# Optimization experiments

Hardware: AMD Instinct MI355X
Metric: run time of the kernel (lower is better)

The kernel has to match this reference:

```python
import jax, jax.numpy as jnp
import numpy as np

SIG_G = [1, 1, 1]          # Clifford signature Cl(3,0): 2^3 = 8 blades
N_BLADES = 1 << len(SIG_G)
LAYER_DIMS = [256, 512, 256]
BATCH = 64
ALPHA = 0.1


def _cayley(g):
    """Cayley table C[a,b,k]: e_a * e_b = C[a,b,a^b] * e_{a^b} (blades as bitmasks)."""
    n = len(g)
    K = 1 << n
    C = np.zeros((K, K, K), dtype=np.float32)
    for a in range(K):
        for b in range(K):
            # canonical reordering sign: count generator swaps
            s, aa = 0, a >> 1
            while aa:
                s += bin(aa & b).count('1')
                aa >>= 1
            sign = -1.0 if (s & 1) else 1.0
            # metric contraction for repeated generators
            for i in range(n):
                if (a >> i) & 1 and (b >> i) & 1:
                    sign *= g[i]
            C[a, b, a ^ b] = sign
    return C


def _reverse_signs(n):
    """Reversion sign per blade: (-1)^{r(r-1)/2} for grade r."""
    K = 1 << n
    r = np.array([bin(k).count('1') for k in range(K)])
    return ((-1.0) ** (r * (r - 1) // 2)).astype(np.float32)


CAYLEY = jnp.asarray(_cayley(SIG_G))          # (K, K, K), sparse signed table
REV = jnp.asarray(_reverse_signs(len(SIG_G)))  # (K,)


def geometric_product(A, W, C):
    # A: (B, N, K) multivectors, W: (M, N, K) multivector weights -> (B, M, K)
    # out[b,m,k] = sum_n sum_{a,c} C[a,c,k] * A[b,n,a] * W[m,n,c]
    return jnp.einsum('bna,mnc,ack->bmk', A, W, C)


def setup_inputs() -> dict:
    key = jax.random.key(0)
    k_x, k_w1, k_w2 = jax.random.split(key, 3)
    x = jax.random.normal(k_x, (BATCH, LAYER_DIMS[0], N_BLADES), dtype=jnp.float32)
    w1 = jax.random.normal(k_w1, (LAYER_DIMS[0], LAYER_DIMS[1], N_BLADES), dtype=jnp.float32) * 0.1
    w2 = jax.random.normal(k_w2, (LAYER_DIMS[1], LAYER_DIMS[2], N_BLADES), dtype=jnp.float32) * 0.1
    return {"x": x, "w1": w1, "w2": w2, "n_iter": 20}


def reference(x, w1, w2, n_iter):
    ws = [w1, w2]
    B = x.shape[0]
    # states[0] is detached input (x.detach().clone() in torch)
    states = [jax.lax.stop_gradient(x)]
    for w in ws:
        states.append(jnp.zeros((B, w.shape[1], N_BLADES), dtype=x.dtype))
    for _ in range(n_iter):
        for l in range(1, len(states)):
            w = ws[l - 1]
            x_hat = geometric_product(states[l], w, CAYLEY)          # (B, D_{l-1}, K)
            err = states[l - 1] - x_hat
            w_T = jnp.transpose(w * REV, (1, 0, 2))                  # reverse + transpose
            # torch: grad = -gp(err, w_T); states[l] -= alpha*grad  => += alpha*gp
            states[l] = states[l] + ALPHA * geometric_product(err, w_T, CAYLEY)
    return tuple(states)
```

## Files before the change

kernel.cpp:

```cpp
#include <hip/hip_runtime.h>

typedef unsigned short u16;
typedef __attribute__((ext_vector_type(4))) float f32x4;
typedef __attribute__((ext_vector_type(8))) __bf16 bf16x8;
typedef __attribute__((ext_vector_type(8))) u16 u16x8;

#define ALPHA_F 0.1f

__device__ __host__ constexpr bool SGN(int a, int c) {
  return ((((c & 1) & (((a >> 1) ^ (a >> 2)) & 1)) ^
           (((c >> 1) & 1) & ((a >> 2) & 1))) != 0);
}
__device__ __host__ constexpr float REVF(int c) {
  const int r = (c & 1) + ((c >> 1) & 1) + ((c >> 2) & 1);
  return (r >= 2) ? -1.f : 1.f;
}
__device__ __forceinline__ u16 bf_rnd(float f) {
  unsigned u = __float_as_uint(f);
  return (u16)((u + 0x7FFFu + ((u >> 16) & 1u)) >> 16);
}
__device__ __forceinline__ float bf_val(u16 h) {
  return __uint_as_float(((unsigned)h) << 16);
}
__device__ __forceinline__ f32x4 mf(bf16x8 a, bf16x8 b, f32x4 c) {
  return __builtin_amdgcn_mfma_f32_16x16x32_bf16(a, b, c, 0, 0, 0);
}
__device__ __forceinline__ bf16x8 negf(bf16x8 v) {
  u16x8 u = __builtin_bit_cast(u16x8, v);
  const u16x8 m = {0x8000, 0x8000, 0x8000, 0x8000, 0x8000, 0x8000, 0x8000, 0x8000};
  u = u ^ m;
  return __builtin_bit_cast(bf16x8, u);
}

__global__ __launch_bounds__(256) void pack_in(
    const float* __restrict__ x, const float* __restrict__ w1,
    const float* __restrict__ w2, u16* P1h, u16* P1l, u16* Q1, u16* Qc1,
    u16* P2h, u16* P2l, u16* Q2, u16* Axh, u16* Axl, u16* Vpk2,
    u16* BpAh, u16* BpAl, u16* Z0h, u16* Z0l, float* out0) {
  const int t = blockIdx.x * 256 + threadIdx.x;
  if (t < 131072) {
    const int r = t >> 9, cc = t & 511;
    const float* s = w1 + ((size_t)r * 512 + cc) * 8;
    float v[8];
#pragma unroll
    for (int c = 0; c < 8; ++c) v[c] = s[c];
    const size_t qo = (size_t)((cc >> 4) * 2 + (r >> 7)) * 32768 +
                      ((r >> 5) & 3) * 512 + ((r >> 3) & 3) * 128 +
                      (cc & 15) * 8 + (r & 7);
#pragma unroll
    for (int c = 0; c < 8; ++c) {
      const float q1 = REVF(c) * v[c];
      u16 h = bf_rnd(q1);
      Q1[qo + c * 4096] = h;
      Q1[qo + c * 4096 + 2048] = bf_rnd(q1 - bf_val(h));
      const float qc = ALPHA_F * q1;
      h = bf_rnd(qc);
      Qc1[qo + c * 4096] = h;
      Qc1[qo + c * 4096 + 2048] = bf_rnd(qc - bf_val(h));
    }
  } else if (t < 262144) {
    const int u = t - 131072;
    const int r = u >> 8, c2 = u & 255;
    const float* s = w2 + ((size_t)r * 256 + c2) * 8;
    float v[8];
#pragma unroll
    for (int c = 0; c < 8; ++c) v[c] = s[c];
    const size_t tail = ((r >> 5) & 3) * 512 + ((r >> 3) & 3) * 128 +
                        (c2 & 15) * 8 + (r & 7);
    const size_t qo = (size_t)((c2 >> 4) * 4 + (r >> 7)) * 32768 + tail;
    const size_t wo = (size_t)((c2 >> 4) * 6 + 2 + (r >> 7)) * 32768 + tail;
#pragma unroll
    for (int c = 0; c < 8; ++c) {
      const float q2 = REVF(c) * v[c];
      u16 h = bf_rnd(q2);
      Q2[qo + c * 4096] = h;
      Q2[qo + c * 4096 + 2048] = bf_rnd(q2 - bf_val(h));
      const float qw = ALPHA_F * q2;
      h = bf_rnd(qw);
      const u16 lo = bf_rnd(qw - bf_val(h));
      Vpk2[wo + c * 4096] = h;
      Vpk2[wo + c * 4096 + 2048] = lo;
      const size_t bo = ((size_t)(c * 32 + (c2 >> 3)) * 512 + r) * 8 + (c2 & 7);
      BpAh[bo] = h;
      BpAl[bo] = lo;
    }
  } else if (t < 393216) {
    const int u = t - 262144;
    const int r = u & 255, cc = u >> 8;
    const float* s = w1 + ((size_t)r * 512 + cc) * 8;
#pragma unroll
    for (int a = 0; a < 8; ++a) {
      const float v = s[a];
      const u16 h = bf_rnd(v);
      const size_t o = ((size_t)(a * 32 + (r >> 3)) * 512 + cc) * 8 + (r & 7);
      P1h[o] = h;
      P1l[o] = bf_rnd(v - bf_val(h));
    }
  } else if (t < 524288) {
    const int u = t - 393216;
    const int r = u & 511, c2 = u >> 9;
    const float* s = w2 + ((size_t)r * 256 + c2) * 8;
#pragma unroll
    for (int a = 0; a < 8; ++a) {
      const float v = s[a];
      const u16 h = bf_rnd(v);
      const size_t o = ((size_t)(a * 64 + (r >> 3)) * 256 + c2) * 8 + (r & 7);
      P2h[o] = h;
      P2l[o] = bf_rnd(v - bf_val(h));
    }
  } else if (t < 540672) {
    const int u = t - 524288;
    const int b = u >> 8, n = u & 255;
    const float* s = x + ((size_t)b * 256 + n) * 8;
#pragma unroll
    for (int a = 0; a < 8; ++a) {
      const u16 h = bf_rnd(s[a]);
      const size_t o = ((size_t)(a * 32 + (n >> 3)) * 64 + b) * 8 + (n & 7);
      Axh[o] = h;
      Axl[o] = bf_rnd(s[a] - bf_val(h));
    }
  } else if (t < 573440) {
    const int u = t - 540672;
    ((float4*)out0)[u] = ((const float4*)x)[u];
  } else if (t < 606208) {
    const int u = t - 573440;
    const int hl = u >> 14, i = u & 16383;
    const int a = i >> 11, j = i & 2047;
    const u16x8 z = {0, 0, 0, 0, 0, 0, 0, 0};
    u16* Z = hl ? Z0l : Z0h;
    *(u16x8*)&Z[(size_t)a * 49152 + (size_t)j * 8] = z;
  }
}

__global__ __launch_bounds__(512, 2) void composeK(
    const u16* __restrict__ P1h, const u16* __restrict__ P1l,
    const u16* __restrict__ Q1, const u16* __restrict__ P2h,
    const u16* __restrict__ P2l, const u16* __restrict__ Q2,
    const u16* __restrict__ Axh, const u16* __restrict__ Axl,
    const u16* __restrict__ Qc1, u16* Vpk1, u16* Vpk2,
    u16* V1pAh, u16* V1pAl, u16* UpAh, u16* UpAl,
    u16* Z0h, u16* Z0l, float* c1Z) {
  __shared__ float pan[8][2176];

  const int bid = blockIdx.x, tid = threadIdx.x;
  const int w = tid >> 6, l = tid & 63;
  const int lg = l >> 4, lm = l & 15;

  int seg, rb, p;
  if (bid < 256) { seg = 1; rb = bid & 15; p = bid >> 4; }
  else if (bid < 1280) { seg = 0; rb = (bid - 256) & 31; p = (bid - 256) >> 5; }
  else { seg = 2; rb = (bid - 1280) & 3; p = (bid - 1280) >> 2; }

  const u16* Ah_ = seg == 0 ? P1h : (seg == 1 ? P2h : Axh);
  const u16* Al_ = seg == 0 ? P1l : (seg == 1 ? P2l : Axl);
  const u16* Vb = seg == 0 ? Q1 : (seg == 1 ? Q2 : Qc1);
  const int NROW = seg == 0 ? 512 : (seg == 1 ? 256 : 64);
  const int KC = seg == 1 ? 64 : 32;
  const int NW = seg == 1 ? 2 : 1;
  const int slmul = seg == 1 ? 4 : 2;
  const int row = rb * 16 + lm;

  f32x4 acc[8];
#pragma unroll
  for (int k = 0; k < 8; ++k) acc[k] = f32x4{0.f, 0.f, 0.f, 0.f};

  for (int wi = 0; wi < NW; ++wi) {
    const int n0 = w * (NW * 32) + wi * 32;
    const int sl = n0 >> 7, hst = (n0 >> 5) & 3;
    const u16* Vimg =
        Vb + ((size_t)(p * slmul + sl) << 15) + hst * 512 + lg * 128 + lm * 8;
    const int kc = (n0 >> 3) + lg;
    bf16x8 ah[8], al[8];
#pragma unroll
    for (int a = 0; a < 8; ++a) {
      const size_t o = ((size_t)(a * KC + kc) * NROW + row) * 8;
      ah[a] = *(const bf16x8*)(Ah_ + o);
      al[a] = *(const bf16x8*)(Al_ + o);
    }
    __builtin_amdgcn_s_setprio(1);
#pragma unroll
    for (int c = 0; c < 8; ++c) {
      const bf16x8 vhp = *(const bf16x8*)(Vimg + (size_t)c * 4096);
      const bf16x8 vlp = *(const bf16x8*)(Vimg + (size_t)c * 4096 + 2048);
      const bf16x8 vhn = negf(vhp), vln = negf(vlp);
#pragma unroll
      for (int a = 0; a < 8; ++a) {
        const int k = a ^ c;
        const bf16x8 vh = SGN(a, c) ? vhn : vhp;
        const bf16x8 vl = SGN(a, c) ? vln : vlp;
        acc[k] = mf(ah[a], vh, acc[k]);
        acc[k] = mf(al[a], vh, acc[k]);
        acc[k] = mf(ah[a], vl, acc[k]);
      }
    }
    __builtin_amdgcn_s_setprio(0);
  }

#pragma unroll
  for (int k = 0; k < 8; ++k)
#pragma unroll
    for (int q = 0; q < 4; ++q)
      pan[w][(k * 16 + lg * 4 + q) * 17 + lm] = acc[k][q];
  __syncthreads();

  if (tid < 256) {
    const int k = tid >> 5, rw = (tid >> 1) & 15, ch = tid & 1;
    const int boff = (k * 16 + rw) * 17 + ch * 8;
    f32x4 s0 = {0.f, 0.f, 0.f, 0.f}, s1 = {0.f, 0.f, 0.f, 0.f};
    for (int ss = 0; ss < 8; ++ss) {
      s0 += *(const f32x4*)&pan[ss][boff];
      s1 += *(const f32x4*)&pan[ss][boff + 4];
    }
    float v[8];
#pragma unroll
    for (int e = 0; e < 4; ++e) { v[e] = s0[e]; v[4 + e] = s1[e]; }
    const int n = rb * 16 + rw;

    if (seg <= 1) {
      u16* base = seg == 0 ? Vpk1 : Vpk2;
      const int blk = (seg == 0 ? p * 4 : p * 6) + (n >> 7);
      u16* d = base + ((size_t)blk << 15) + (size_t)k * 4096 +
               ((n >> 5) & 3) * 512 + ((n >> 3) & 3) * 128 + (n & 7);
      u16 ph[8], pl[8];
#pragma unroll
      for (int e = 0; e < 8; ++e) {
        const int m = p * 16 + ch * 8 + e;
        const float val = ((k == 0) && (n == m) ? 1.0f : 0.0f) - ALPHA_F * v[e];
        const u16 hh = bf_rnd(val);
        const u16 ll = bf_rnd(val - bf_val(hh));
        d[(size_t)(ch * 8 + e) * 8] = hh;
        d[2048 + (size_t)(ch * 8 + e) * 8] = ll;
        ph[e] = hh;
        pl[e] = ll;
      }
      if (seg == 0) {
        const size_t po = (((size_t)k * 64 + p * 2 + ch) * 512 + n) * 8;
        *(u16x8*)&V1pAh[po] = *(u16x8*)ph;
        *(u16x8*)&V1pAl[po] = *(u16x8*)pl;
      } else {
        const size_t po = (((size_t)k * 32 + p * 2 + ch) * 256 + n) * 8;
        *(u16x8*)&UpAh[po] = *(u16x8*)ph;
        *(u16x8*)&UpAl[po] = *(u16x8*)pl;
      }
    } else {
      const int b = n;
      float* cp_ = c1Z + (((size_t)k * 64 + p * 2 + ch) * 64 + b) * 8;
      u16x8 h8, l8;
#pragma unroll
      for (int e = 0; e < 8; ++e) {
        cp_[e] = v[e];
        const u16 hh = bf_rnd(v[e]);
        h8[e] = hh;
        l8[e] = bf_rnd(v[e] - bf_val(hh));
      }
      const size_t zo = (((size_t)k * 96 + 32 + p * 2 + ch) * 64 + b) * 8;
      *(u16x8*)&Z0h[zo] = h8;
      *(u16x8*)&Z0l[zo] = l8;
    }
  }
}

__global__ __launch_bounds__(512, 2) void compose2(
    const u16* __restrict__ V1pAh, const u16* __restrict__ V1pAl,
    const u16* __restrict__ UpAh, const u16* __restrict__ UpAl,
    const u16* __restrict__ BpAh, const u16* __restrict__ BpAl,
    const u16* __restrict__ Vpk1, const u16* __restrict__ Wcat,
    u16* V1sqI, u16* Wcat2) {
  __shared__ float pan[8][2176];

  const int bid = blockIdx.x, tid = threadIdx.x;
  const int w = tid >> 6, l = tid & 63;
  const int lg = l >> 4, lm = l & 15;

  int seg, rb, p;
  if (bid < 1024) { seg = 0; rb = bid & 31; p = bid >> 5; }
  else if (bid < 1536) { seg = 1; rb = (bid - 1024) & 31; p = (bid - 1024) >> 5; }
  else { seg = 2; rb = (bid - 1536) & 15; p = (bid - 1536) >> 4; }

  const int nwin = seg == 0 ? 2 : (seg == 1 ? 3 : 1);
  const int row = rb * 16 + lm;

  f32x4 acc[8];
#pragma unroll
  for (int k = 0; k < 8; ++k) acc[k] = f32x4{0.f, 0.f, 0.f, 0.f};

  for (int wi = 0; wi < nwin; ++wi) {
    const int g = w * nwin + wi;
    const u16 *Aph, *Apl;
    int AKC, AR, kcb;
    const u16* Vimg;
    if (seg == 0) {
      Aph = V1pAh; Apl = V1pAl; AKC = 64; AR = 512; kcb = g * 4;
      Vimg = Vpk1 + ((size_t)(p * 4 + (g >> 2)) << 15) + (g & 3) * 512;
    } else if (seg == 1) {
      if (g < 8) {
        Aph = BpAh; Apl = BpAl; AKC = 32; AR = 512; kcb = g * 4;
        Vimg = Wcat + ((size_t)(p * 6 + (g >> 2)) << 15) + (g & 3) * 512;
      } else {
        const int g2_ = g - 8;
        Aph = V1pAh; Apl = V1pAl; AKC = 64; AR = 512; kcb = g2_ * 4;
        Vimg = Wcat + ((size_t)(p * 6 + 2 + (g2_ >> 2)) << 15) + (g2_ & 3) * 512;
      }
    } else {
      Aph = UpAh; Apl = UpAl; AKC = 32; AR = 256; kcb = g * 4;
      Vimg = Wcat + ((size_t)(p * 6 + (g >> 2)) << 15) + (g & 3) * 512;
    }
    Vimg += lg * 128 + lm * 8;
    const int kc = kcb + lg;
    bf16x8 ah[8], al[8];
#pragma unroll
    for (int a = 0; a < 8; ++a) {
      const size_t o = ((size_t)(a * AKC + kc) * AR + row) * 8;
      ah[a] = *(const bf16x8*)(Aph + o);
      al[a] = *(const bf16x8*)(Apl + o);
    }
    __builtin_amdgcn_s_setprio(1);
#pragma unroll
    for (int c = 0; c < 8; ++c) {
      const bf16x8 vhp = *(const bf16x8*)(Vimg + (size_t)c * 4096);
      const bf16x8 vlp = *(const bf16x8*)(Vimg + (size_t)c * 4096 + 2048);
      const bf16x8 vhn = negf(vhp), vln = negf(vlp);
#pragma unroll
      for (int a = 0; a < 8; ++a) {
        const int k = a ^ c;
        const bf16x8 vh = SGN(a, c) ? vhn : vhp;
        const bf16x8 vl = SGN(a, c) ? vln : vlp;
        acc[k] = mf(ah[a], vh, acc[k]);
        acc[k] = mf(al[a], vh, acc[k]);
        acc[k] = mf(ah[a], vl, acc[k]);
      }
    }
    __builtin_amdgcn_s_setprio(0);
  }

#pragma unroll
  for (int k = 0; k < 8; ++k)
#pragma unroll
    for (int q = 0; q < 4; ++q)
      pan[w][(k * 16 + lg * 4 + q) * 17 + lm] = acc[k][q];
  __syncthreads();

  if (tid < 256) {
    const int k = tid >> 5, rw = (tid >> 1) & 15, ch = tid & 1;
    const int boff = (k * 16 + rw) * 17 + ch * 8;
    f32x4 s0 = {0.f, 0.f, 0.f, 0.f}, s1 = {0.f, 0.f, 0.f, 0.f};
    for (int ss = 0; ss < 8; ++ss) {
      s0 += *(const f32x4*)&pan[ss][boff];
      s1 += *(const f32x4*)&pan[ss][boff + 4];
    }
    float v[8];
#pragma unroll
    for (int e = 0; e < 4; ++e) { v[e] = s0[e]; v[4 + e] = s1[e]; }
    const int n = rb * 16 + rw;

    u16* base = seg == 0 ? V1sqI : Wcat2;
    int blk;
    if (seg == 0) blk = p * 4 + (n >> 7);
    else if (seg == 1) blk = p * 6 + 2 + (n >> 7);
    else blk = p * 6 + (n >> 7);
    u16* d = base + ((size_t)blk << 15) + (size_t)k * 4096 +
             ((n >> 5) & 3) * 512 + ((n >> 3) & 3) * 128 + (n & 7);
#pragma unroll
    for (int e = 0; e < 8; ++e) {
      const float val = v[e];
      const u16 hh = bf_rnd(val);
      d[(size_t)(ch * 8 + e) * 8] = hh;
      d[2048 + (size_t)(ch * 8 + e) * 8] = bf_rnd(val - bf_val(hh));
    }
  }
}

struct IArgs {
  const u16 *Zch, *Zcl;
  u16 *Znh, *Znl;
  const u16 *V1, *V2;
  const float *add1, *add2;
  float *oa1, *oa2;
  float *out1, *out2;
  int n_g1;
};

template <bool G1>
__device__ __forceinline__ void iter_body(const IArgs& A, int t18, int fin,
                                          float (*pan)[2176]) {
  const int bid = blockIdx.x, tid = threadIdx.x;
  const int w = tid >> 6, l = tid & 63;
  const int lg = l >> 4, lm = l & 15;
  const int rb = G1 ? bid : bid - A.n_g1;
  constexpr int NPAN = G1 ? 32 : 16;
  const int p = rb & (NPAN - 1);
  const int bh = rb / NPAN;
  const int b0 = bh * 16;
  constexpr int KW = G1 ? 64 : 96;
  constexpr int NW = G1 ? 2 : 3;
  constexpr int acb0 = G1 ? 32 : 0;
  constexpr int slmul = G1 ? 4 : 6;
  const u16* Vb = G1 ? A.V1 : A.V2;

  f32x4 acc[8];
#pragma unroll
  for (int k = 0; k < 8; ++k) acc[k] = f32x4{0.f, 0.f, 0.f, 0.f};

#pragma unroll
  for (int wi = 0; wi < NW; ++wi) {
    const int n0 = w * KW + wi * 32;
    const int sl = n0 >> 7, hst = (n0 >> 5) & 3;
    const u16* Vimg = Vb + ((size_t)(p * slmul + sl) << 15) + hst * 512 +
                      lg * 128 + lm * 8;
    const size_t ao = ((size_t)(acb0 + (n0 >> 3) + lg) * 64 + b0 + lm) * 8;
    bf16x8 ah[8], al[8];
#pragma unroll
    for (int a = 0; a < 8; ++a) {
      ah[a] = *(const bf16x8*)(A.Zch + (size_t)a * 49152 + ao);
      al[a] = *(const bf16x8*)(A.Zcl + (size_t)a * 49152 + ao);
    }
    __builtin_amdgcn_s_setprio(1);
#pragma unroll
    for (int c = 0; c < 8; ++c) {
      const bf16x8 vhp = *(const bf16x8*)(Vimg + (size_t)c * 4096);
      const bf16x8 vlp = *(const bf16x8*)(Vimg + (size_t)c * 4096 + 2048);
      const bf16x8 vhn = negf(vhp), vln = negf(vlp);
#pragma unroll
      for (int a = 0; a < 8; ++a) {
        const int k = a ^ c;
        const bf16x8 vh = SGN(a, c) ? vhn : vhp;
        const bf16x8 vl = SGN(a, c) ? vln : vlp;
        acc[k] = mf(ah[a], vh, acc[k]);
        acc[k] = mf(al[a], vh, acc[k]);
        acc[k] = mf(ah[a], vl, acc[k]);
      }
    }
    __builtin_amdgcn_s_setprio(0);
  }

#pragma unroll
  for (int k = 0; k < 8; ++k)
#pragma unroll
    for (int q = 0; q < 4; ++q)
      pan[w][(k * 16 + lg * 4 + q) * 17 + lm] = acc[k][q];
  __syncthreads();

  if (tid < 256) {
    const int k = tid >> 5, row = (tid >> 1) & 15, ch = tid & 1;
    const int boff = (k * 16 + row) * 17 + ch * 8;
    f32x4 s0 = {0.f, 0.f, 0.f, 0.f}, s1 = {0.f, 0.f, 0.f, 0.f};
    for (int ss = 0; ss < 8; ++ss) {
      s0 += *(const f32x4*)&pan[ss][boff];
      s1 += *(const f32x4*)&pan[ss][boff + 4];
    }
    const int b = b0 + row;
    if constexpr (G1) {
      if (A.add1) {
        const float* ca = A.add1 + (((size_t)k * 64 + p * 2 + ch) * 64 + b) * 8;
        s0 += *(const f32x4*)ca;
        s1 += *(const f32x4*)(ca + 4);
      }
    } else {
      if (A.add2) {
        const float* ca = A.add2 + (((size_t)k * 32 + p * 2 + ch) * 64 + b) * 8;
        s0 += *(const f32x4*)ca;
        s1 += *(const f32x4*)(ca + 4);
      }
    }
    float v[8];
#pragma unroll
    for (int e = 0; e < 4; ++e) { v[e] = s0[e]; v[4 + e] = s1[e]; }
    if constexpr (G1) {
      if (A.oa1) {
        float* q = A.oa1 + (((size_t)k * 64 + p * 2 + ch) * 64 + b) * 8;
#pragma unroll
        for (int e = 0; e < 8; ++e) q[e] = v[e];
      }
    } else {
      if (A.oa2) {
        float* q = A.oa2 + (((size_t)k * 32 + p * 2 + ch) * 64 + b) * 8;
#pragma unroll
        for (int e = 0; e < 8; ++e) q[e] = v[e];
      }
    }
    if (!fin) {
      u16x8 h8, l8;
#pragma unroll
      for (int e = 0; e < 8; ++e) {
        const u16 hh = bf_rnd(v[e]);
        h8[e] = hh;
        l8[e] = bf_rnd(v[e] - bf_val(hh));
      }
      const size_t zo =
          (((size_t)k * 96 + (G1 ? 32 : 0) + p * 2 + ch) * 64 + b) * 8;
      *(u16x8*)&A.Znh[zo] = h8;
      *(u16x8*)&A.Znl[zo] = l8;
    }
    if constexpr (G1) {
      if (t18) {
#pragma unroll
        for (int e = 0; e < 8; ++e)
          A.out1[((size_t)b * 512 + p * 16 + ch * 8 + e) * 8 + k] = v[e];
      }
    } else {
      if (fin) {
#pragma unroll
        for (int e = 0; e < 8; ++e)
          A.out2[((size_t)b * 256 + p * 16 + ch * 8 + e) * 8 + k] = v[e];
      }
    }
  }
}

__global__ __launch_bounds__(512, 2) void iter_k(IArgs A, int t18, int fin) {
  __shared__ float pan[8][2176];
  if ((int)blockIdx.x < A.n_g1) iter_body<true>(A, t18, fin, pan);
  else iter_body<false>(A, t18, fin, pan);
}

extern "C" void kernel_launch(void* const* d_in, const int* in_sizes, int n_in,
                              void* d_out, int out_size, void* d_ws,
                              size_t ws_size, hipStream_t stream) {
  const float* x = (const float*)d_in[0];
  const float* w1 = (const float*)d_in[1];
  const float* w2 = (const float*)d_in[2];

  float* out0 = (float*)d_out;
  float* out1 = out0 + 131072;
  float* out2 = out1 + 262144;

  char* W = (char*)d_ws;
  const size_t MB = 1ull << 20;
  u16* Vpk1 = (u16*)(W);
  u16* Wcat = (u16*)(W + 8 * MB);
  u16* Q1 = (u16*)(W + 14 * MB);
  u16* Q2 = (u16*)(W + 18 * MB);
  u16* Qc1 = (u16*)(W + 22 * MB);
  u16* P1h = (u16*)(W + 26 * MB);
  u16* P1l = (u16*)(W + 28 * MB);
  u16* P2h = (u16*)(W + 30 * MB);
  u16* P2l = (u16*)(W + 32 * MB);
  u16* Axh = (u16*)(W + 34 * MB);
  u16* Axl = (u16*)(W + 34 * MB + 262144);
  float* c1Z = (float*)(W + 35 * MB);
  u16* V1sqI = (u16*)(W + 36 * MB);
  u16* Wcat2 = (u16*)(W + 44 * MB);
  u16* V1pAh = (u16*)(W + 50 * MB);
  u16* V1pAl = (u16*)(W + 54 * MB);
  u16* UpAh = (u16*)(W + 58 * MB);
  u16* UpAl = (u16*)(W + 59 * MB);
  u16* BpAh = (u16*)(W + 60 * MB);
  u16* BpAl = (u16*)(W + 62 * MB);
  float* c1bZ = (float*)(W + 64 * MB);
  float* d2Z = (float*)(W + 65 * MB);
  u16* Z0h = (u16*)(W + 66 * MB);
  u16* Z0l = Z0h + 393216;
  u16* Z1h = Z0h + 786432;
  u16* Z1l = Z0h + 1179648;

  pack_in<<<2368, 256, 0, stream>>>(x, w1, w2, P1h, P1l, Q1, Qc1, P2h, P2l, Q2,
                                    Axh, Axl, Wcat, BpAh, BpAl, Z0h, Z0l, out0);

  composeK<<<1408, 512, 0, stream>>>(P1h, P1l, Q1, P2h, P2l, Q2, Axh, Axl, Qc1,
                                     Vpk1, Wcat, V1pAh, V1pAl, UpAh, UpAl,
                                     Z0h, Z0l, c1Z);

  compose2<<<1792, 512, 0, stream>>>(V1pAh, V1pAl, UpAh, UpAl, BpAh, BpAl,
                                     Vpk1, Wcat, V1sqI, Wcat2);

  {
    IArgs ia{Z0h, Z0l, Z1h, Z1l, Vpk1, Wcat, c1Z, nullptr,
             c1bZ, d2Z, out1, out2, 128};
    iter_k<<<192, 512, 0, stream>>>(ia, 0, 0);
  }

  for (int tau = 0; tau < 9; ++tau) {
    const bool odd = tau & 1;
    IArgs ia{odd ? Z0h : Z1h, odd ? Z0l : Z1l,
             odd ? Z1h : Z0h, odd ? Z1l : Z0l,
             V1sqI, Wcat2, c1bZ, d2Z, nullptr, nullptr, out1, out2, 128};
    iter_k<<<192, 512, 0, stream>>>(ia, tau == 8 ? 1 : 0, 0);
  }

  {
    IArgs ia{Z0h, Z0l, Z1h, Z1l, Vpk1, Wcat, nullptr, nullptr,
             nullptr, nullptr, out1, out2, 0};
    iter_k<<<64, 512, 0, stream>>>(ia, 0, 1);
  }
}
```

Before: 363.0 us.

## Fuse compose2 with first iteration kernel and double row tile for seg0

```diff
diff --git a/kernel.cpp b/kernel.cpp
--- a/kernel.cpp
+++ b/kernel.cpp
@@ -260,116 +260,6 @@
   }
 }
 
-__global__ __launch_bounds__(512, 2) void compose2(
-    const u16* __restrict__ V1pAh, const u16* __restrict__ V1pAl,
-    const u16* __restrict__ UpAh, const u16* __restrict__ UpAl,
-    const u16* __restrict__ BpAh, const u16* __restrict__ BpAl,
-    const u16* __restrict__ Vpk1, const u16* __restrict__ Wcat,
-    u16* V1sqI, u16* Wcat2) {
-  __shared__ float pan[8][2176];
-
-  const int bid = blockIdx.x, tid = threadIdx.x;
-  const int w = tid >> 6, l = tid & 63;
-  const int lg = l >> 4, lm = l & 15;
-
-  int seg, rb, p;
-  if (bid < 1024) { seg = 0; rb = bid & 31; p = bid >> 5; }
-  else if (bid < 1536) { seg = 1; rb = (bid - 1024) & 31; p = (bid - 1024) >> 5; }
-  else { seg = 2; rb = (bid - 1536) & 15; p = (bid - 1536) >> 4; }
-
-  const int nwin = seg == 0 ? 2 : (seg == 1 ? 3 : 1);
-  const int row = rb * 16 + lm;
-
-  f32x4 acc[8];
-#pragma unroll
-  for (int k = 0; k < 8; ++k) acc[k] = f32x4{0.f, 0.f, 0.f, 0.f};
-
-  for (int wi = 0; wi < nwin; ++wi) {
-    const int g = w * nwin + wi;
-    const u16 *Aph, *Apl;
-    int AKC, AR, kcb;
-    const u16* Vimg;
-    if (seg == 0) {
-      Aph = V1pAh; Apl = V1pAl; AKC = 64; AR = 512; kcb = g * 4;
-      Vimg = Vpk1 + ((size_t)(p * 4 + (g >> 2)) << 15) + (g & 3) * 512;
-    } else if (seg == 1) {
-      if (g < 8) {
-        Aph = BpAh; Apl = BpAl; AKC = 32; AR = 512; kcb = g * 4;
-        Vimg = Wcat + ((size_t)(p * 6 + (g >> 2)) << 15) + (g & 3) * 512;
-      } else {
-        const int g2_ = g - 8;
-        Aph = V1pAh; Apl = V1pAl; AKC = 64; AR = 512; kcb = g2_ * 4;
-        Vimg = Wcat + ((size_t)(p * 6 + 2 + (g2_ >> 2)) << 15) + (g2_ & 3) * 512;
-      }
-    } else {
-      Aph = UpAh; Apl = UpAl; AKC = 32; AR = 256; kcb = g * 4;
-      Vimg = Wcat + ((size_t)(p * 6 + (g >> 2)) << 15) + (g & 3) * 512;
-    }
-    Vimg += lg * 128 + lm * 8;
-    const int kc = kcb + lg;
-    bf16x8 ah[8], al[8];
-#pragma unroll
-    for (int a = 0; a < 8; ++a) {
-      const size_t o = ((size_t)(a * AKC + kc) * AR + row) * 8;
-      ah[a] = *(const bf16x8*)(Aph + o);
-      al[a] = *(const bf16x8*)(Apl + o);
-    }
-    __builtin_amdgcn_s_setprio(1);
-#pragma unroll
-    for (int c = 0; c < 8; ++c) {
-      const bf16x8 vhp = *(const bf16x8*)(Vimg + (size_t)c * 4096);
-      const bf16x8 vlp = *(const bf16x8*)(Vimg + (size_t)c * 4096 + 2048);
-      const bf16x8 vhn = negf(vhp), vln = negf(vlp);
-#pragma unroll
-      for (int a = 0; a < 8; ++a) {
-        const int k = a ^ c;
-        const bf16x8 vh = SGN(a, c) ? vhn : vhp;
-        const bf16x8 vl = SGN(a, c) ? vln : vlp;
-        acc[k] = mf(ah[a], vh, acc[k]);
-        acc[k] = mf(al[a], vh, acc[k]);
-        acc[k] = mf(ah[a], vl, acc[k]);
-      }
-    }
-    __builtin_amdgcn_s_setprio(0);
-  }
-
-#pragma unroll
-  for (int k = 0; k < 8; ++k)
-#pragma unroll
-    for (int q = 0; q < 4; ++q)
-      pan[w][(k * 16 + lg * 4 + q) * 17 + lm] = acc[k][q];
-  __syncthreads();
-
-  if (tid < 256) {
-    const int k = tid >> 5, rw = (tid >> 1) & 15, ch = tid & 1;
-    const int boff = (k * 16 + rw) * 17 + ch * 8;
-    f32x4 s0 = {0.f, 0.f, 0.f, 0.f}, s1 = {0.f, 0.f, 0.f, 0.f};
-    for (int ss = 0; ss < 8; ++ss) {
-      s0 += *(const f32x4*)&pan[ss][boff];
-      s1 += *(const f32x4*)&pan[ss][boff + 4];
-    }
-    float v[8];
-#pragma unroll
-    for (int e = 0; e < 4; ++e) { v[e] = s0[e]; v[4 + e] = s1[e]; }
-    const int n = rb * 16 + rw;
-
-    u16* base = seg == 0 ? V1sqI : Wcat2;
-    int blk;
-    if (seg == 0) blk = p * 4 + (n >> 7);
-    else if (seg == 1) blk = p * 6 + 2 + (n >> 7);
-    else blk = p * 6 + (n >> 7);
-    u16* d = base + ((size_t)blk << 15) + (size_t)k * 4096 +
-             ((n >> 5) & 3) * 512 + ((n >> 3) & 3) * 128 + (n & 7);
-#pragma unroll
-    for (int e = 0; e < 8; ++e) {
-      const float val = v[e];
-      const u16 hh = bf_rnd(val);
-      d[(size_t)(ch * 8 + e) * 8] = hh;
-      d[2048 + (size_t)(ch * 8 + e) * 8] = bf_rnd(val - bf_val(hh));
-    }
-  }
-}
-
 struct IArgs {
   const u16 *Zch, *Zcl;
   u16 *Znh, *Znl;
@@ -381,12 +271,12 @@
 };
 
 template <bool G1>
-__device__ __forceinline__ void iter_body(const IArgs& A, int t18, int fin,
-                                          float (*pan)[2176]) {
-  const int bid = blockIdx.x, tid = threadIdx.x;
+__device__ __forceinline__ void iter_body(const IArgs& A, int vbid, int t18,
+                                          int fin, float (*pan)[2176]) {
+  const int tid = threadIdx.x;
   const int w = tid >> 6, l = tid & 63;
   const int lg = l >> 4, lm = l & 15;
-  const int rb = G1 ? bid : bid - A.n_g1;
+  const int rb = G1 ? vbid : vbid - A.n_g1;
   constexpr int NPAN = G1 ? 32 : 16;
   const int p = rb & (NPAN - 1);
   const int bh = rb / NPAN;
@@ -509,8 +399,199 @@
 
 __global__ __launch_bounds__(512, 2) void iter_k(IArgs A, int t18, int fin) {
   __shared__ float pan[8][2176];
-  if ((int)blockIdx.x < A.n_g1) iter_body<true>(A, t18, fin, pan);
-  else iter_body<false>(A, t18, fin, pan);
+  if ((int)blockIdx.x < A.n_g1) iter_body<true>(A, blockIdx.x, t18, fin, pan);
+  else iter_body<false>(A, blockIdx.x, t18, fin, pan);
+}
+
+struct C2A {
+  const u16 *V1pAh, *V1pAl, *UpAh, *UpAl, *BpAh, *BpAl;
+  const u16 *Vpk1, *Wcat;
+  u16 *V1sqI, *Wcat2;
+};
+
+__global__ __launch_bounds__(512) void combo(IArgs S, C2A C) {
+  __shared__ float pan[8][2176];
+  const int bid = blockIdx.x, tid = threadIdx.x;
+
+  if (bid < 192) {
+    if (bid < S.n_g1) iter_body<true>(S, bid, 0, 0, pan);
+    else iter_body<false>(S, bid, 0, 0, pan);
+    return;
+  }
+  const int cb = bid - 192;
+  const int w = tid >> 6, l = tid & 63;
+  const int lg = l >> 4, lm = l & 15;
+
+  if (cb < 512) {
+    const int p = cb >> 4, rq = cb & 15;
+    const int row0 = rq * 32 + lm, row1 = row0 + 16;
+    f32x4 acc0[8], acc1[8];
+#pragma unroll
+    for (int k = 0; k < 8; ++k) {
+      acc0[k] = f32x4{0.f, 0.f, 0.f, 0.f};
+      acc1[k] = f32x4{0.f, 0.f, 0.f, 0.f};
+    }
+#pragma unroll
+    for (int wi = 0; wi < 2; ++wi) {
+      const int g = w * 2 + wi;
+      const u16* Vimg = C.Vpk1 + ((size_t)(p * 4 + (g >> 2)) << 15) +
+                        (g & 3) * 512 + lg * 128 + lm * 8;
+      const int kc = g * 4 + lg;
+      bf16x8 a0h[8], a0l[8], a1h[8], a1l[8];
+#pragma unroll
+      for (int a = 0; a < 8; ++a) {
+        const size_t o0 = ((size_t)(a * 64 + kc) * 512 + row0) * 8;
+        const size_t o1 = ((size_t)(a * 64 + kc) * 512 + row1) * 8;
+        a0h[a] = *(const bf16x8*)(C.V1pAh + o0);
+        a0l[a] = *(const bf16x8*)(C.V1pAl + o0);
+        a1h[a] = *(const bf16x8*)(C.V1pAh + o1);
+        a1l[a] = *(const bf16x8*)(C.V1pAl + o1);
+      }
+      __builtin_amdgcn_s_setprio(1);
+#pragma unroll
+      for (int c = 0; c < 8; ++c) {
+        const bf16x8 vhp = *(const bf16x8*)(Vimg + (size_t)c * 4096);
+        const bf16x8 vlp = *(const bf16x8*)(Vimg + (size_t)c * 4096 + 2048);
+        const bf16x8 vhn = negf(vhp), vln = negf(vlp);
+#pragma unroll
+        for (int a = 0; a < 8; ++a) {
+          const int k = a ^ c;
+          const bf16x8 vh = SGN(a, c) ? vhn : vhp;
+          const bf16x8 vl = SGN(a, c) ? vln : vlp;
+          acc0[k] = mf(a0h[a], vh, acc0[k]);
+          acc0[k] = mf(a0l[a], vh, acc0[k]);
+          acc0[k] = mf(a0h[a], vl, acc0[k]);
+          acc1[k] = mf(a1h[a], vh, acc1[k]);
+          acc1[k] = mf(a1l[a], vh, acc1[k]);
+          acc1[k] = mf(a1h[a], vl, acc1[k]);
+        }
+      }
+      __builtin_amdgcn_s_setprio(0);
+    }
+#pragma unroll
+    for (int rg = 0; rg < 2; ++rg) {
+#pragma unroll
+      for (int k = 0; k < 8; ++k)
+#pragma unroll
+        for (int q = 0; q < 4; ++q)
+          pan[w][(k * 16 + lg * 4 + q) * 17 + lm] =
+              rg ? acc1[k][q] : acc0[k][q];
+      __syncthreads();
+      if (tid < 256) {
+        const int k = tid >> 5, rw = (tid >> 1) & 15, ch = tid & 1;
+        const int boff = (k * 16 + rw) * 17 + ch * 8;
+        f32x4 s0 = {0.f, 0.f, 0.f, 0.f}, s1 = {0.f, 0.f, 0.f, 0.f};
+        for (int ss = 0; ss < 8; ++ss) {
+          s0 += *(const f32x4*)&pan[ss][boff];
+          s1 += *(const f32x4*)&pan[ss][boff + 4];
+        }
+        float v[8];
+#pragma unroll
+        for (int e = 0; e < 4; ++e) { v[e] = s0[e]; v[4 + e] = s1[e]; }
+        const int n = rq * 32 + rg * 16 + rw;
+        const int blk = p * 4 + (n >> 7);
+        u16* d = C.V1sqI + ((size_t)blk << 15) + (size_t)k * 4096 +
+                 ((n >> 5) & 3) * 512 + ((n >> 3) & 3) * 128 + (n & 7);
+#pragma unroll
+        for (int e = 0; e < 8; ++e) {
+          const float val = v[e];
+          const u16 hh = bf_rnd(val);
+          d[(size_t)(ch * 8 + e) * 8] = hh;
+          d[2048 + (size_t)(ch * 8 + e) * 8] = bf_rnd(val - bf_val(hh));
+        }
+      }
+      __syncthreads();
+    }
+    return;
+  }
+
+  int seg, rb, p;
+  if (cb < 1024) { seg = 1; rb = (cb - 512) & 31; p = (cb - 512) >> 5; }
+  else { seg = 2; rb = (cb - 1024) & 15; p = (cb - 1024) >> 4; }
+  const int nwin = seg == 1 ? 3 : 1;
+  const int row = rb * 16 + lm;
+
+  f32x4 acc[8];
+#pragma unroll
+  for (int k = 0; k < 8; ++k) acc[k] = f32x4{0.f, 0.f, 0.f, 0.f};
+
+  for (int wi = 0; wi < nwin; ++wi) {
+    const int g = w * nwin + wi;
+    const u16 *Aph, *Apl;
+    int AKC, AR, kcb;
+    const u16* Vimg;
+    if (seg == 1) {
+      if (g < 8) {
+        Aph = C.BpAh; Apl = C.BpAl; AKC = 32; AR = 512; kcb = g * 4;
+        Vimg = C.Wcat + ((size_t)(p * 6 + (g >> 2)) << 15) + (g & 3) * 512;
+      } else {
+        const int g2_ = g - 8;
+        Aph = C.V1pAh; Apl = C.V1pAl; AKC = 64; AR = 512; kcb = g2_ * 4;
+        Vimg = C.Wcat + ((size_t)(p * 6 + 2 + (g2_ >> 2)) << 15) + (g2_ & 3) * 512;
+      }
+    } else {
+      Aph = C.UpAh; Apl = C.UpAl; AKC = 32; AR = 256; kcb = g * 4;
+      Vimg = C.Wcat + ((size_t)(p * 6 + (g >> 2)) << 15) + (g & 3) * 512;
+    }
+    Vimg += lg * 128 + lm * 8;
+    const int kc = kcb + lg;
+    bf16x8 ah[8], al[8];
+#pragma unroll
+    for (int a = 0; a < 8; ++a) {
+      const size_t o = ((size_t)(a * AKC + kc) * AR + row) * 8;
+      ah[a] = *(const bf16x8*)(Aph + o);
+      al[a] = *(const bf16x8*)(Apl + o);
+    }
+    __builtin_amdgcn_s_setprio(1);
+#pragma unroll
+    for (int c = 0; c < 8; ++c) {
+      const bf16x8 vhp = *(const bf16x8*)(Vimg + (size_t)c * 4096);
+      const bf16x8 vlp = *(const bf16x8*)(Vimg + (size_t)c * 4096 + 2048);
+      const bf16x8 vhn = negf(vhp), vln = negf(vlp);
+#pragma unroll
+      for (int a = 0; a < 8; ++a) {
+        const int k = a ^ c;
+        const bf16x8 vh = SGN(a, c) ? vhn : vhp;
+        const bf16x8 vl = SGN(a, c) ? vln : vlp;
+        acc[k] = mf(ah[a], vh, acc[k]);
+        acc[k] = mf(al[a], vh, acc[k]);
+        acc[k] = mf(ah[a], vl, acc[k]);
+      }
+    }
+    __builtin_amdgcn_s_setprio(0);
+  }
+
+#pragma unroll
+  for (int k = 0; k < 8; ++k)
+#pragma unroll
+    for (int q = 0; q < 4; ++q)
+      pan[w][(k * 16 + lg * 4 + q) * 17 + lm] = acc[k][q];
+  __syncthreads();
+
+  if (tid < 256) {
+    const int k = tid >> 5, rw = (tid >> 1) & 15, ch = tid & 1;
+    const int boff = (k * 16 + rw) * 17 + ch * 8;
+    f32x4 s0 = {0.f, 0.f, 0.f, 0.f}, s1 = {0.f, 0.f, 0.f, 0.f};
+    for (int ss = 0; ss < 8; ++ss) {
+      s0 += *(const f32x4*)&pan[ss][boff];
+      s1 += *(const f32x4*)&pan[ss][boff + 4];
+    }
+    float v[8];
+#pragma unroll
+    for (int e = 0; e < 4; ++e) { v[e] = s0[e]; v[4 + e] = s1[e]; }
+    const int n = rb * 16 + rw;
+
+    const int blk = seg == 1 ? (p * 6 + 2 + (n >> 7)) : (p * 6 + (n >> 7));
+    u16* d = C.Wcat2 + ((size_t)blk << 15) + (size_t)k * 4096 +
+             ((n >> 5) & 3) * 512 + ((n >> 3) & 3) * 128 + (n & 7);
+#pragma unroll
+    for (int e = 0; e < 8; ++e) {
+      const float val = v[e];
+      const u16 hh = bf_rnd(val);
+      d[(size_t)(ch * 8 + e) * 8] = hh;
+      d[2048 + (size_t)(ch * 8 + e) * 8] = bf_rnd(val - bf_val(hh));
+    }
+  }
 }
 
 extern "C" void kernel_launch(void* const* d_in, const int* in_sizes, int n_in,
@@ -560,13 +641,11 @@
                                      Vpk1, Wcat, V1pAh, V1pAl, UpAh, UpAl,
                                      Z0h, Z0l, c1Z);
 
-  compose2<<<1792, 512, 0, stream>>>(V1pAh, V1pAl, UpAh, UpAl, BpAh, BpAl,
-                                     Vpk1, Wcat, V1sqI, Wcat2);
-
   {
-    IArgs ia{Z0h, Z0l, Z1h, Z1l, Vpk1, Wcat, c1Z, nullptr,
-             c1bZ, d2Z, out1, out2, 128};
-    iter_k<<<192, 512, 0, stream>>>(ia, 0, 0);
+    IArgs seed{Z0h, Z0l, Z1h, Z1l, Vpk1, Wcat, c1Z, nullptr,
+               c1bZ, d2Z, out1, out2, 128};
+    C2A c2{V1pAh, V1pAl, UpAh, UpAl, BpAh, BpAl, Vpk1, Wcat, V1sqI, Wcat2};
+    combo<<<1472, 512, 0, stream>>>(seed, c2);
   }
 
   for (int tau = 0; tau < 9; ++tau) {
```

Result: faster. 354.6 us (-2.3%).
